# Kernel optimization log

Hardware: AMD Instinct MI355X
Metric: run time of the kernel (lower is better)

## Reference

```python
import jax, jax.numpy as jnp
import numpy as np

GH, GW, B, H, OUT = 9, 9, 1024, 256, 1


def setup_inputs() -> dict:
    key = jax.random.key(0)
    ks = jax.random.split(key, 16)
    N = GH * GW
    s3 = 1.0 / np.sqrt(3 * H)
    sH = 1.0 / np.sqrt(H)
    return {
        "x": jax.random.normal(ks[0], (B, GH, GW), jnp.float32),
        "h_ext": jax.random.normal(ks[1], (B, H), jnp.float32),
        "c_ext": jax.random.normal(ks[2], (B, H), jnp.float32),
        "grid_h": jax.random.normal(ks[3], (GH, GW, B, H), jnp.float32),
        "grid_c": jax.random.normal(ks[4], (GH, GW, B, H), jnp.float32),
        "W_hp": jax.random.normal(ks[5], (N, H, 3 * H), jnp.float32) * s3,
        "b_hp": jax.random.normal(ks[6], (N, H), jnp.float32) * s3,
        "W_cp": jax.random.normal(ks[7], (N, H, 3 * H), jnp.float32) * s3,
        "b_cp": jax.random.normal(ks[8], (N, H), jnp.float32) * s3,
        "W_ih": jax.random.normal(ks[9], (N, 4 * H, 1), jnp.float32) * sH,
        "W_hh": jax.random.normal(ks[10], (N, 4 * H, H), jnp.float32) * sH,
        "b_ih": jax.random.normal(ks[11], (N, 4 * H), jnp.float32) * sH,
        "b_hh": jax.random.normal(ks[12], (N, 4 * H), jnp.float32) * sH,
        "W_out": jax.random.normal(ks[13], (OUT, H), jnp.float32) * sH,
        "b_out": jnp.zeros((OUT,), jnp.float32),
    }


def _lstm_cell(x_cell, h0, c0, W_ih_k, W_hh_k, b_ih_k, b_hh_k):
    # x_cell: [B,1], h0/c0: [B,H]; torch LSTMCell math
    gates = x_cell @ W_ih_k.T + b_ih_k + h0 @ W_hh_k.T + b_hh_k  # [B,4H]
    i, f, g, o = jnp.split(gates, 4, axis=1)
    i, f, o = jax.nn.sigmoid(i), jax.nn.sigmoid(f), jax.nn.sigmoid(o)
    g = jnp.tanh(g)
    c = f * c0 + i * g
    h = o * jnp.tanh(c)
    return h, c


def reference(x, h_ext, c_ext, grid_h, grid_c,
              W_hp, b_hp, W_cp, b_cp,
              W_ih, W_hh, b_ih, b_hh, W_out, b_out):
    zeros = jnp.zeros((B, H), x.dtype)
    # new states, updated in raster order; left/up neighbors read NEW states
    new_h = [[None] * GW for _ in range(GH)]
    new_c = [[None] * GW for _ in range(GH)]
    for i in range(GH):
        for j in range(GW):
            k = i * GW + j
            h_prev, c_prev = grid_h[i, j], grid_c[i, j]
            if i == 0 and j == 0:
                h_left, c_left = h_ext, c_ext
            elif j > 0:
                h_left, c_left = new_h[i][j - 1], new_c[i][j - 1]
            else:
                h_left, c_left = zeros, zeros
            if i > 0:
                h_up, c_up = new_h[i - 1][j], new_c[i - 1][j]
            else:
                h_up, c_up = zeros, zeros
            comb_h = jnp.concatenate([h_left, h_up, h_prev], axis=1)  # [B,3H]
            comb_c = jnp.concatenate([c_left, c_up, c_prev], axis=1)
            ph = comb_h @ W_hp[k].T + b_hp[k]
            pc = comb_c @ W_cp[k].T + b_cp[k]
            x_cell = x[:, i, j][:, None]  # [B,1]
            h_new, c_new = _lstm_cell(x_cell, ph, pc, W_ih[k], W_hh[k], b_ih[k], b_hh[k])
            new_h[i][j], new_c[i][j] = h_new, c_new
    final_h, final_c = new_h[-1][-1], new_c[-1][-1]
    # fc_out with fc_layers_out=[0]: Linear + ReLU, then sigmoid
    out = jax.nn.sigmoid(jax.nn.relu(final_h @ W_out.T + b_out))
    gh = jnp.stack([jnp.stack(r, 0) for r in new_h], 0)
    gc = jnp.stack([jnp.stack(r, 0) for r in new_c], 0)
    return out, final_h, final_c, gh, gc
```

## Files before the change

### kernel.cpp

```cpp
#include <hip/hip_runtime.h>
#include <math.h>

#define BATCH 1024
#define HID 256

typedef __bf16 bf16_t;
typedef __bf16 bf16x8 __attribute__((ext_vector_type(8)));
typedef float f32x4 __attribute__((ext_vector_type(4)));

struct ProjDesc {
    const float* left;
    const float* up;
    const float* prev;
    const float* W;
    const float* bias;
    float* out;
};
struct ProjBatchArgs { ProjDesc d[18]; };

struct CellDesc {
    const float* ph;
    const float* pc;
    const float* Whh;
    const float* Wih;
    const float* bih;
    const float* bhh;
    const float* xcol;
    float* gh;
    float* gc;
};
struct CellBatchArgs { CellDesc d[9]; };

__device__ inline bf16x8 cvt8(const float4 a, const float4 b) {
    bf16x8 r;
    r[0] = (bf16_t)a.x; r[1] = (bf16_t)a.y; r[2] = (bf16_t)a.z; r[3] = (bf16_t)a.w;
    r[4] = (bf16_t)b.x; r[5] = (bf16_t)b.y; r[6] = (bf16_t)b.z; r[7] = (bf16_t)b.w;
    return r;
}

__global__ __launch_bounds__(256) void proj_kernel(ProjBatchArgs args) {
    const ProjDesc pd = args.d[blockIdx.z];
    __shared__ bf16_t Asm[128][40];
    __shared__ bf16_t Bsm[128][40];
    const int t = threadIdx.x;
    const int lane = t & 63, wid = t >> 6;
    const int wm = wid & 1, wn = wid >> 1;
    const int ln = lane & 15, lh = lane >> 4;
    const int b0 = blockIdx.x * 128;
    const int n0 = blockIdx.y * 128;
    const int sr = t >> 1, sq = (t & 1) * 16;

    const float* aSeg[3]; int kOff[3]; int nseg = 0;
    if (pd.left) { aSeg[nseg] = pd.left; kOff[nseg] = 0;   ++nseg; }
    if (pd.up)   { aSeg[nseg] = pd.up;   kOff[nseg] = 256; ++nseg; }
    aSeg[nseg] = pd.prev; kOff[nseg] = 512; ++nseg;
    const int iters = nseg * 8;

    const size_t aoff = (size_t)(b0 + sr) * HID + sq;
    const float* wbase = pd.W + (size_t)(n0 + sr) * (3 * HID) + sq;

    f32x4 acc[4][4] = {};
    float4 sa[4], sb[4];
    {
        const float* ap = aSeg[0] + aoff;
        const float* wp = wbase + kOff[0];
        #pragma unroll
        for (int m = 0; m < 4; ++m) sa[m] = *(const float4*)(ap + m * 4);
        #pragma unroll
        for (int m = 0; m < 4; ++m) sb[m] = *(const float4*)(wp + m * 4);
    }
    for (int i = 0; i < iters; ++i) {
        const bf16x8 av0 = cvt8(sa[0], sa[1]), av1 = cvt8(sa[2], sa[3]);
        const bf16x8 bv0 = cvt8(sb[0], sb[1]), bv1 = cvt8(sb[2], sb[3]);
        __syncthreads();
        *(bf16x8*)&Asm[sr][sq] = av0;
        *(bf16x8*)&Asm[sr][sq + 8] = av1;
        *(bf16x8*)&Bsm[sr][sq] = bv0;
        *(bf16x8*)&Bsm[sr][sq + 8] = bv1;
        __syncthreads();
        if (i + 1 < iters) {
            const int s = (i + 1) >> 3, kb = (i + 1) & 7;
            const float* ap = aSeg[s] + aoff + kb * 32;
            const float* wp = wbase + kOff[s] + kb * 32;
            #pragma unroll
            for (int m = 0; m < 4; ++m) sa[m] = *(const float4*)(ap + m * 4);
            #pragma unroll
            for (int m = 0; m < 4; ++m) sb[m] = *(const float4*)(wp + m * 4);
        }
        bf16x8 af[4], bfv[4];
        #pragma unroll
        for (int mf = 0; mf < 4; ++mf)
            af[mf] = *(const bf16x8*)&Asm[wm * 64 + mf * 16 + ln][lh * 8];
        #pragma unroll
        for (int nf = 0; nf < 4; ++nf)
            bfv[nf] = *(const bf16x8*)&Bsm[wn * 64 + nf * 16 + ln][lh * 8];
        #pragma unroll
        for (int mf = 0; mf < 4; ++mf)
            #pragma unroll
            for (int nf = 0; nf < 4; ++nf)
                acc[mf][nf] = __builtin_amdgcn_mfma_f32_16x16x32_bf16(
                    af[mf], bfv[nf], acc[mf][nf], 0, 0, 0);
    }
    #pragma unroll
    for (int nf = 0; nf < 4; ++nf) {
        const int n = n0 + wn * 64 + nf * 16 + ln;
        const float bias = pd.bias[n];
        #pragma unroll
        for (int mf = 0; mf < 4; ++mf)
            #pragma unroll
            for (int r = 0; r < 4; ++r) {
                const int b = b0 + wm * 64 + mf * 16 + lh * 4 + r;
                pd.out[(size_t)b * HID + n] = acc[mf][nf][r] + bias;
            }
    }
}

__global__ __launch_bounds__(256) void cell_kernel(CellBatchArgs args) {
    const CellDesc cd = args.d[blockIdx.z];
    __shared__ bf16_t Psm[128][40];
    __shared__ bf16_t Wsm[128][40];
    const int t = threadIdx.x;
    const int lane = t & 63, wid = t >> 6;
    const int wm = wid & 1, wn = wid >> 1;
    const int ln = lane & 15, lh = lane >> 4;
    const int b0 = blockIdx.x * 128;
    const int u0 = blockIdx.y * 32;
    const int sr = t >> 1, sq = (t & 1) * 16;

    const float* pbase = cd.ph + (size_t)(b0 + sr) * HID + sq;
    const int cg = sr >> 5, cdu = sr & 31;
    const float* wbase = cd.Whh + (size_t)(cg * HID + u0 + cdu) * HID + sq;

    f32x4 acc[4][4] = {};
    float4 sa[4], sb[4];
    #pragma unroll
    for (int m = 0; m < 4; ++m) sa[m] = *(const float4*)(pbase + m * 4);
    #pragma unroll
    for (int m = 0; m < 4; ++m) sb[m] = *(const float4*)(wbase + m * 4);

    for (int kb = 0; kb < 8; ++kb) {
        const bf16x8 pv0 = cvt8(sa[0], sa[1]), pv1 = cvt8(sa[2], sa[3]);
        const bf16x8 wv0 = cvt8(sb[0], sb[1]), wv1 = cvt8(sb[2], sb[3]);
        __syncthreads();
        *(bf16x8*)&Psm[sr][sq] = pv0;
        *(bf16x8*)&Psm[sr][sq + 8] = pv1;
        *(bf16x8*)&Wsm[sr][sq] = wv0;
        *(bf16x8*)&Wsm[sr][sq + 8] = wv1;
        __syncthreads();
        if (kb + 1 < 8) {
            #pragma unroll
            for (int m = 0; m < 4; ++m) sa[m] = *(const float4*)(pbase + (kb + 1) * 32 + m * 4);
            #pragma unroll
            for (int m = 0; m < 4; ++m) sb[m] = *(const float4*)(wbase + (kb + 1) * 32 + m * 4);
        }
        bf16x8 af[4], bfr[4];
        #pragma unroll
        for (int mf = 0; mf < 4; ++mf)
            af[mf] = *(const bf16x8*)&Psm[wm * 64 + mf * 16 + ln][lh * 8];
        #pragma unroll
        for (int g = 0; g < 4; ++g)
            bfr[g] = *(const bf16x8*)&Wsm[g * 32 + wn * 16 + ln][lh * 8];
        #pragma unroll
        for (int mf = 0; mf < 4; ++mf)
            #pragma unroll
            for (int g = 0; g < 4; ++g)
                acc[mf][g] = __builtin_amdgcn_mfma_f32_16x16x32_bf16(
                    af[mf], bfr[g], acc[mf][g], 0, 0, 0);
    }

    const int u = u0 + wn * 16 + ln;
    float wih[4], bsum[4];
    #pragma unroll
    for (int g = 0; g < 4; ++g) {
        const int n = g * HID + u;
        wih[g] = cd.Wih[n];
        bsum[g] = cd.bih[n] + cd.bhh[n];
    }
    #pragma unroll
    for (int mf = 0; mf < 4; ++mf)
        #pragma unroll
        for (int r = 0; r < 4; ++r) {
            const int b = b0 + wm * 64 + mf * 16 + lh * 4 + r;
            const float xv = cd.xcol[(size_t)b * 81];
            const float gi = acc[mf][0][r] + xv * wih[0] + bsum[0];
            const float gf = acc[mf][1][r] + xv * wih[1] + bsum[1];
            const float gg = acc[mf][2][r] + xv * wih[2] + bsum[2];
            const float go = acc[mf][3][r] + xv * wih[3] + bsum[3];
            const float i_ = 1.f / (1.f + expf(-gi));
            const float f_ = 1.f / (1.f + expf(-gf));
            const float o_ = 1.f / (1.f + expf(-go));
            const float g_ = tanhf(gg);
            const float c0 = cd.pc[(size_t)b * HID + u];
            const float cn = f_ * c0 + i_ * g_;
            const float hn = o_ * tanhf(cn);
            cd.gh[(size_t)b * HID + u] = hn;
            cd.gc[(size_t)b * HID + u] = cn;
        }
}

__global__ __launch_bounds__(256) void final_kernel(
        const float* __restrict__ gh88, const float* __restrict__ gc88,
        const float* __restrict__ Wout, const float* __restrict__ bout,
        float* __restrict__ out, float* __restrict__ fh, float* __restrict__ fc) {
    const int tid = blockIdx.x * blockDim.x + threadIdx.x;
    const int nth = gridDim.x * blockDim.x;
    for (int idx = tid; idx < BATCH * HID; idx += nth) {
        fh[idx] = gh88[idx];
        fc[idx] = gc88[idx];
    }
    if (tid < BATCH) {
        float s = bout[0];
        for (int k = 0; k < HID; ++k) s += gh88[(size_t)tid * HID + k] * Wout[k];
        s = fmaxf(s, 0.f);
        out[tid] = 1.f / (1.f + expf(-s));
    }
}

extern "C" void kernel_launch(void* const* d_in, const int* in_sizes, int n_in,
                              void* d_out, int out_size, void* d_ws, size_t ws_size,
                              hipStream_t stream) {
    const float* x      = (const float*)d_in[0];
    const float* h_ext  = (const float*)d_in[1];
    const float* c_ext  = (const float*)d_in[2];
    const float* grid_h = (const float*)d_in[3];
    const float* grid_c = (const float*)d_in[4];
    const float* W_hp   = (const float*)d_in[5];
    const float* b_hp   = (const float*)d_in[6];
    const float* W_cp   = (const float*)d_in[7];
    const float* b_cp   = (const float*)d_in[8];
    const float* W_ih   = (const float*)d_in[9];
    const float* W_hh   = (const float*)d_in[10];
    const float* b_ih   = (const float*)d_in[11];
    const float* b_hh   = (const float*)d_in[12];
    const float* W_out  = (const float*)d_in[13];
    const float* b_out  = (const float*)d_in[14];

    float* out = (float*)d_out;
    float* fh  = out + BATCH * 1;
    float* fc  = fh + BATCH * HID;
    float* gh  = fc + BATCH * HID;
    float* gc  = gh + (size_t)81 * BATCH * HID;

    float* ws = (float*)d_ws;

    for (int d = 0; d <= 16; ++d) {
        const int i_lo = d > 8 ? d - 8 : 0;
        const int i_hi = d < 8 ? d : 8;
        const int nc = i_hi - i_lo + 1;
        ProjBatchArgs pa{};
        CellBatchArgs ca{};
        for (int s = 0; s < nc; ++s) {
            const int i = i_lo + s, j = d - i;
            const int k = i * 9 + j;
            const float *hl, *cl, *hu, *cu;
            if (i == 0 && j == 0)      { hl = h_ext; cl = c_ext; }
            else if (j > 0)            { hl = gh + (size_t)(k - 1) * BATCH * HID;
                                         cl = gc + (size_t)(k - 1) * BATCH * HID; }
            else                       { hl = nullptr; cl = nullptr; }
            if (i > 0)                 { hu = gh + (size_t)(k - 9) * BATCH * HID;
                                         cu = gc + (size_t)(k - 9) * BATCH * HID; }
            else                       { hu = nullptr; cu = nullptr; }
            const float* hp = grid_h + (size_t)k * BATCH * HID;
            const float* cp = grid_c + (size_t)k * BATCH * HID;
            float* ph = ws + (size_t)s * 2 * BATCH * HID;
            float* pc = ph + BATCH * HID;
            pa.d[2 * s + 0] = { hl, hu, hp, W_hp + (size_t)k * HID * 3 * HID,
                                b_hp + (size_t)k * HID, ph };
            pa.d[2 * s + 1] = { cl, cu, cp, W_cp + (size_t)k * HID * 3 * HID,
                                b_cp + (size_t)k * HID, pc };
            ca.d[s] = { ph, pc,
                        W_hh + (size_t)k * 4 * HID * HID,
                        W_ih + (size_t)k * 4 * HID,
                        b_ih + (size_t)k * 4 * HID,
                        b_hh + (size_t)k * 4 * HID,
                        x + i * 9 + j,
                        gh + (size_t)k * BATCH * HID,
                        gc + (size_t)k * BATCH * HID };
        }
        proj_kernel<<<dim3(8, 2, 2 * nc), 256, 0, stream>>>(pa);
        cell_kernel<<<dim3(8, 8, nc), 256, 0, stream>>>(ca);
    }
    final_kernel<<<dim3(64), 256, 0, stream>>>(
        gh + (size_t)80 * BATCH * HID, gc + (size_t)80 * BATCH * HID,
        W_out, b_out, out, fh, fc);
}
```

Baseline: 1.151 ms.

## Hoist prev-state projections out of the wavefront and split-K with atomics

Projections of the grid's previous state do not depend on the wavefront, so all 81 cells' h/c prev-projections (plus bias) are now computed up front in one large launch. Each diagonal then only runs the left and up K-segments, as separate blocks that atomically add into the precomputed outputs. This takes a third of the K work off the serial critical path and adds parallelism per diagonal. In exchange it needs a 162-slot workspace (with a fallback path when the workspace is smaller), uses float atomics that make summation order nondeterministic, and drops the register prefetch double-buffering in the GEMM loops.

```diff
diff --git a/kernel.cpp b/kernel.cpp
--- a/kernel.cpp
+++ b/kernel.cpp
@@ -3,33 +3,12 @@
 
 #define BATCH 1024
 #define HID 256
+#define W3 768
+#define SLOT (BATCH * HID)
 
 typedef __bf16 bf16_t;
 typedef __bf16 bf16x8 __attribute__((ext_vector_type(8)));
 typedef float f32x4 __attribute__((ext_vector_type(4)));
-
-struct ProjDesc {
-    const float* left;
-    const float* up;
-    const float* prev;
-    const float* W;
-    const float* bias;
-    float* out;
-};
-struct ProjBatchArgs { ProjDesc d[18]; };
-
-struct CellDesc {
-    const float* ph;
-    const float* pc;
-    const float* Whh;
-    const float* Wih;
-    const float* bih;
-    const float* bhh;
-    const float* xcol;
-    float* gh;
-    float* gc;
-};
-struct CellBatchArgs { CellDesc d[9]; };
 
 __device__ inline bf16x8 cvt8(const float4 a, const float4 b) {
     bf16x8 r;
@@ -38,55 +17,37 @@
     return r;
 }
 
-__global__ __launch_bounds__(256) void proj_kernel(ProjBatchArgs args) {
-    const ProjDesc pd = args.d[blockIdx.z];
-    __shared__ bf16_t Asm[128][40];
-    __shared__ bf16_t Bsm[128][40];
+template<bool ATOMIC>
+__device__ __forceinline__ void proj_core(
+        const float* __restrict__ src, const float* __restrict__ W, int koff,
+        const float* __restrict__ bias, float* __restrict__ out,
+        bf16_t (*Asm)[40], bf16_t (*Bsm)[40]) {
     const int t = threadIdx.x;
     const int lane = t & 63, wid = t >> 6;
     const int wm = wid & 1, wn = wid >> 1;
     const int ln = lane & 15, lh = lane >> 4;
-    const int b0 = blockIdx.x * 128;
-    const int n0 = blockIdx.y * 128;
+    const int b0 = blockIdx.x * 128, n0 = blockIdx.y * 128;
     const int sr = t >> 1, sq = (t & 1) * 16;
-
-    const float* aSeg[3]; int kOff[3]; int nseg = 0;
-    if (pd.left) { aSeg[nseg] = pd.left; kOff[nseg] = 0;   ++nseg; }
-    if (pd.up)   { aSeg[nseg] = pd.up;   kOff[nseg] = 256; ++nseg; }
-    aSeg[nseg] = pd.prev; kOff[nseg] = 512; ++nseg;
-    const int iters = nseg * 8;
-
-    const size_t aoff = (size_t)(b0 + sr) * HID + sq;
-    const float* wbase = pd.W + (size_t)(n0 + sr) * (3 * HID) + sq;
-
+    const float* arow = src + (size_t)(b0 + sr) * HID + sq;
+    const float* wrow = W + (size_t)(n0 + sr) * W3 + koff + sq;
     f32x4 acc[4][4] = {};
-    float4 sa[4], sb[4];
-    {
-        const float* ap = aSeg[0] + aoff;
-        const float* wp = wbase + kOff[0];
-        #pragma unroll
-        for (int m = 0; m < 4; ++m) sa[m] = *(const float4*)(ap + m * 4);
-        #pragma unroll
-        for (int m = 0; m < 4; ++m) sb[m] = *(const float4*)(wp + m * 4);
-    }
-    for (int i = 0; i < iters; ++i) {
-        const bf16x8 av0 = cvt8(sa[0], sa[1]), av1 = cvt8(sa[2], sa[3]);
-        const bf16x8 bv0 = cvt8(sb[0], sb[1]), bv1 = cvt8(sb[2], sb[3]);
+    for (int kb = 0; kb < 8; ++kb) {
+        const float4 a0 = *(const float4*)(arow + kb * 32);
+        const float4 a1 = *(const float4*)(arow + kb * 32 + 4);
+        const float4 a2 = *(const float4*)(arow + kb * 32 + 8);
+        const float4 a3 = *(const float4*)(arow + kb * 32 + 12);
+        const float4 w0 = *(const float4*)(wrow + kb * 32);
+        const float4 w1 = *(const float4*)(wrow + kb * 32 + 4);
+        const float4 w2 = *(const float4*)(wrow + kb * 32 + 8);
+        const float4 w3 = *(const float4*)(wrow + kb * 32 + 12);
+        const bf16x8 av0 = cvt8(a0, a1), av1 = cvt8(a2, a3);
+        const bf16x8 bv0 = cvt8(w0, w1), bv1 = cvt8(w2, w3);
         __syncthreads();
         *(bf16x8*)&Asm[sr][sq] = av0;
         *(bf16x8*)&Asm[sr][sq + 8] = av1;
         *(bf16x8*)&Bsm[sr][sq] = bv0;
         *(bf16x8*)&Bsm[sr][sq + 8] = bv1;
         __syncthreads();
-        if (i + 1 < iters) {
-            const int s = (i + 1) >> 3, kb = (i + 1) & 7;
-            const float* ap = aSeg[s] + aoff + kb * 32;
-            const float* wp = wbase + kOff[s] + kb * 32;
-            #pragma unroll
-            for (int m = 0; m < 4; ++m) sa[m] = *(const float4*)(ap + m * 4);
-            #pragma unroll
-            for (int m = 0; m < 4; ++m) sb[m] = *(const float4*)(wp + m * 4);
-        }
         bf16x8 af[4], bfv[4];
         #pragma unroll
         for (int mf = 0; mf < 4; ++mf)
@@ -104,16 +65,52 @@
     #pragma unroll
     for (int nf = 0; nf < 4; ++nf) {
         const int n = n0 + wn * 64 + nf * 16 + ln;
-        const float bias = pd.bias[n];
+        const float bn = ATOMIC ? 0.f : bias[n];
         #pragma unroll
         for (int mf = 0; mf < 4; ++mf)
             #pragma unroll
             for (int r = 0; r < 4; ++r) {
                 const int b = b0 + wm * 64 + mf * 16 + lh * 4 + r;
-                pd.out[(size_t)b * HID + n] = acc[mf][nf][r] + bias;
+                if (ATOMIC)
+                    unsafeAtomicAdd(out + (size_t)b * HID + n, acc[mf][nf][r]);
+                else
+                    out[(size_t)b * HID + n] = acc[mf][nf][r] + bn;
             }
     }
 }
+
+__global__ __launch_bounds__(256) void prevproj_kernel(
+        const float* __restrict__ gridh, const float* __restrict__ gridc,
+        const float* __restrict__ Whp, const float* __restrict__ Wcp,
+        const float* __restrict__ bhp, const float* __restrict__ bcp,
+        float* __restrict__ pall) {
+    __shared__ bf16_t As[128][40];
+    __shared__ bf16_t Bs[128][40];
+    const int z = blockIdx.z, k = z >> 1, hc = z & 1;
+    const float* src = (hc ? gridc : gridh) + (size_t)k * SLOT;
+    const float* W = (hc ? Wcp : Whp) + (size_t)k * HID * W3;
+    const float* bias = (hc ? bcp : bhp) + (size_t)k * HID;
+    proj_core<false>(src, W, 512, bias, pall + (size_t)z * SLOT, As, Bs);
+}
+
+struct SegDesc { const float* src; const float* W; const float* bias; float* out; int koff; };
+struct SegArgs { SegDesc d[36]; };
+
+__global__ __launch_bounds__(256) void projseg_kernel(SegArgs a) {
+    __shared__ bf16_t As[128][40];
+    __shared__ bf16_t Bs[128][40];
+    const SegDesc d = a.d[blockIdx.z];
+    if (d.bias) proj_core<false>(d.src, d.W, d.koff, d.bias, d.out, As, Bs);
+    else        proj_core<true>(d.src, d.W, d.koff, nullptr, d.out, As, Bs);
+}
+
+struct CellDesc {
+    const float* ph; const float* pc;
+    const float* Whh; const float* Wih; const float* bih; const float* bhh;
+    const float* xcol;
+    float* gh; float* gc;
+};
+struct CellBatchArgs { CellDesc d[9]; };
 
 __global__ __launch_bounds__(256) void cell_kernel(CellBatchArgs args) {
     const CellDesc cd = args.d[blockIdx.z];
@@ -126,33 +123,28 @@
     const int b0 = blockIdx.x * 128;
     const int u0 = blockIdx.y * 32;
     const int sr = t >> 1, sq = (t & 1) * 16;
-
-    const float* pbase = cd.ph + (size_t)(b0 + sr) * HID + sq;
+    const float* prow = cd.ph + (size_t)(b0 + sr) * HID + sq;
     const int cg = sr >> 5, cdu = sr & 31;
-    const float* wbase = cd.Whh + (size_t)(cg * HID + u0 + cdu) * HID + sq;
+    const float* wrow = cd.Whh + (size_t)(cg * HID + u0 + cdu) * HID + sq;
 
     f32x4 acc[4][4] = {};
-    float4 sa[4], sb[4];
-    #pragma unroll
-    for (int m = 0; m < 4; ++m) sa[m] = *(const float4*)(pbase + m * 4);
-    #pragma unroll
-    for (int m = 0; m < 4; ++m) sb[m] = *(const float4*)(wbase + m * 4);
-
     for (int kb = 0; kb < 8; ++kb) {
-        const bf16x8 pv0 = cvt8(sa[0], sa[1]), pv1 = cvt8(sa[2], sa[3]);
-        const bf16x8 wv0 = cvt8(sb[0], sb[1]), wv1 = cvt8(sb[2], sb[3]);
+        const float4 p0 = *(const float4*)(prow + kb * 32);
+        const float4 p1 = *(const float4*)(prow + kb * 32 + 4);
+        const float4 p2 = *(const float4*)(prow + kb * 32 + 8);
+        const float4 p3 = *(const float4*)(prow + kb * 32 + 12);
+        const float4 w0 = *(const float4*)(wrow + kb * 32);
+        const float4 w1 = *(const float4*)(wrow + kb * 32 + 4);
+        const float4 w2 = *(const float4*)(wrow + kb * 32 + 8);
+        const float4 w3 = *(const float4*)(wrow + kb * 32 + 12);
+        const bf16x8 pv0 = cvt8(p0, p1), pv1 = cvt8(p2, p3);
+        const bf16x8 wv0 = cvt8(w0, w1), wv1 = cvt8(w2, w3);
         __syncthreads();
         *(bf16x8*)&Psm[sr][sq] = pv0;
         *(bf16x8*)&Psm[sr][sq + 8] = pv1;
         *(bf16x8*)&Wsm[sr][sq] = wv0;
         *(bf16x8*)&Wsm[sr][sq + 8] = wv1;
         __syncthreads();
-        if (kb + 1 < 8) {
-            #pragma unroll
-            for (int m = 0; m < 4; ++m) sa[m] = *(const float4*)(pbase + (kb + 1) * 32 + m * 4);
-            #pragma unroll
-            for (int m = 0; m < 4; ++m) sb[m] = *(const float4*)(wbase + (kb + 1) * 32 + m * 4);
-        }
         bf16x8 af[4], bfr[4];
         #pragma unroll
         for (int mf = 0; mf < 4; ++mf)
@@ -237,50 +229,96 @@
 
     float* out = (float*)d_out;
     float* fh  = out + BATCH * 1;
-    float* fc  = fh + BATCH * HID;
-    float* gh  = fc + BATCH * HID;
-    float* gc  = gh + (size_t)81 * BATCH * HID;
+    float* fc  = fh + SLOT;
+    float* gh  = fc + SLOT;
+    float* gc  = gh + (size_t)81 * SLOT;
 
     float* ws = (float*)d_ws;
-
-    for (int d = 0; d <= 16; ++d) {
-        const int i_lo = d > 8 ? d - 8 : 0;
-        const int i_hi = d < 8 ? d : 8;
-        const int nc = i_hi - i_lo + 1;
-        ProjBatchArgs pa{};
-        CellBatchArgs ca{};
-        for (int s = 0; s < nc; ++s) {
-            const int i = i_lo + s, j = d - i;
-            const int k = i * 9 + j;
-            const float *hl, *cl, *hu, *cu;
-            if (i == 0 && j == 0)      { hl = h_ext; cl = c_ext; }
-            else if (j > 0)            { hl = gh + (size_t)(k - 1) * BATCH * HID;
-                                         cl = gc + (size_t)(k - 1) * BATCH * HID; }
-            else                       { hl = nullptr; cl = nullptr; }
-            if (i > 0)                 { hu = gh + (size_t)(k - 9) * BATCH * HID;
-                                         cu = gc + (size_t)(k - 9) * BATCH * HID; }
-            else                       { hu = nullptr; cu = nullptr; }
-            const float* hp = grid_h + (size_t)k * BATCH * HID;
-            const float* cp = grid_c + (size_t)k * BATCH * HID;
-            float* ph = ws + (size_t)s * 2 * BATCH * HID;
-            float* pc = ph + BATCH * HID;
-            pa.d[2 * s + 0] = { hl, hu, hp, W_hp + (size_t)k * HID * 3 * HID,
-                                b_hp + (size_t)k * HID, ph };
-            pa.d[2 * s + 1] = { cl, cu, cp, W_cp + (size_t)k * HID * 3 * HID,
-                                b_cp + (size_t)k * HID, pc };
-            ca.d[s] = { ph, pc,
-                        W_hh + (size_t)k * 4 * HID * HID,
-                        W_ih + (size_t)k * 4 * HID,
-                        b_ih + (size_t)k * 4 * HID,
-                        b_hh + (size_t)k * 4 * HID,
-                        x + i * 9 + j,
-                        gh + (size_t)k * BATCH * HID,
-                        gc + (size_t)k * BATCH * HID };
+    const bool bigws = ws_size >= (size_t)162 * SLOT * 4;
+
+    if (bigws) {
+        prevproj_kernel<<<dim3(8, 2, 162), 256, 0, stream>>>(
+            grid_h, grid_c, W_hp, W_cp, b_hp, b_cp, ws);
+        for (int d = 0; d <= 16; ++d) {
+            const int i_lo = d > 8 ? d - 8 : 0;
+            const int i_hi = d < 8 ? d : 8;
+            const int nc = i_hi - i_lo + 1;
+            SegArgs sa{};
+            CellBatchArgs ca{};
+            int nd = 0;
+            for (int s = 0; s < nc; ++s) {
+                const int i = i_lo + s, j = d - i;
+                const int k = i * 9 + j;
+                float* oh = ws + (size_t)(2 * k) * SLOT;
+                float* oc = oh + SLOT;
+                const float* Wh = W_hp + (size_t)k * HID * W3;
+                const float* Wc = W_cp + (size_t)k * HID * W3;
+                if (i == 0 && j == 0) {
+                    sa.d[nd++] = { h_ext, Wh, nullptr, oh, 0 };
+                    sa.d[nd++] = { c_ext, Wc, nullptr, oc, 0 };
+                } else if (j > 0) {
+                    sa.d[nd++] = { gh + (size_t)(k - 1) * SLOT, Wh, nullptr, oh, 0 };
+                    sa.d[nd++] = { gc + (size_t)(k - 1) * SLOT, Wc, nullptr, oc, 0 };
+                }
+                if (i > 0) {
+                    sa.d[nd++] = { gh + (size_t)(k - 9) * SLOT, Wh, nullptr, oh, 256 };
+                    sa.d[nd++] = { gc + (size_t)(k - 9) * SLOT, Wc, nullptr, oc, 256 };
+                }
+                ca.d[s] = { oh, oc,
+                            W_hh + (size_t)k * 4 * HID * HID,
+                            W_ih + (size_t)k * 4 * HID,
+                            b_ih + (size_t)k * 4 * HID,
+                            b_hh + (size_t)k * 4 * HID,
+                            x + i * 9 + j,
+                            gh + (size_t)k * SLOT,
+                            gc + (size_t)k * SLOT };
+            }
+            projseg_kernel<<<dim3(8, 2, nd), 256, 0, stream>>>(sa);
+            cell_kernel<<<dim3(8, 8, nc), 256, 0, stream>>>(ca);
         }
-        proj_kernel<<<dim3(8, 2, 2 * nc), 256, 0, stream>>>(pa);
-        cell_kernel<<<dim3(8, 8, nc), 256, 0, stream>>>(ca);
+    } else {
+        for (int d = 0; d <= 16; ++d) {
+            const int i_lo = d > 8 ? d - 8 : 0;
+            const int i_hi = d < 8 ? d : 8;
+            const int nc = i_hi - i_lo + 1;
+            SegArgs base{}, inc{};
+            CellBatchArgs ca{};
+            int nb = 0, ni = 0;
+            for (int s = 0; s < nc; ++s) {
+                const int i = i_lo + s, j = d - i;
+                const int k = i * 9 + j;
+                float* oh = ws + (size_t)(2 * s) * SLOT;
+                float* oc = oh + SLOT;
+                const float* Wh = W_hp + (size_t)k * HID * W3;
+                const float* Wc = W_cp + (size_t)k * HID * W3;
+                base.d[nb++] = { grid_h + (size_t)k * SLOT, Wh, b_hp + (size_t)k * HID, oh, 512 };
+                base.d[nb++] = { grid_c + (size_t)k * SLOT, Wc, b_cp + (size_t)k * HID, oc, 512 };
+                if (i == 0 && j == 0) {
+                    inc.d[ni++] = { h_ext, Wh, nullptr, oh, 0 };
+                    inc.d[ni++] = { c_ext, Wc, nullptr, oc, 0 };
+                } else if (j > 0) {
+                    inc.d[ni++] = { gh + (size_t)(k - 1) * SLOT, Wh, nullptr, oh, 0 };
+                    inc.d[ni++] = { gc + (size_t)(k - 1) * SLOT, Wc, nullptr, oc, 0 };
+                }
+                if (i > 0) {
+                    inc.d[ni++] = { gh + (size_t)(k - 9) * SLOT, Wh, nullptr, oh, 256 };
+                    inc.d[ni++] = { gc + (size_t)(k - 9) * SLOT, Wc, nullptr, oc, 256 };
+                }
+                ca.d[s] = { oh, oc,
+                            W_hh + (size_t)k * 4 * HID * HID,
+                            W_ih + (size_t)k * 4 * HID,
+                            b_ih + (size_t)k * 4 * HID,
+                            b_hh + (size_t)k * 4 * HID,
+                            x + i * 9 + j,
+                            gh + (size_t)k * SLOT,
+                            gc + (size_t)k * SLOT };
+            }
+            projseg_kernel<<<dim3(8, 2, nb), 256, 0, stream>>>(base);
+            projseg_kernel<<<dim3(8, 2, ni), 256, 0, stream>>>(inc);
+            cell_kernel<<<dim3(8, 8, nc), 256, 0, stream>>>(ca);
+        }
     }
     final_kernel<<<dim3(64), 256, 0, stream>>>(
-        gh + (size_t)80 * BATCH * HID, gc + (size_t)80 * BATCH * HID,
+        gh + (size_t)80 * SLOT, gc + (size_t)80 * SLOT,
         W_out, b_out, out, fh, fc);
 }
```

Result: faster. 1.095 ms (-4.9%).
